# Kernel optimization log

Measured on AMD Instinct MI355X. Metric: run time of the kernel, lower is better.

## Reference

```python
import jax, jax.numpy as jnp
import numpy as np

B, N, D, DK = 8, 2048, 1024, 64
GAMMA = 0.001

def setup_inputs() -> dict:
    key = jax.random.key(0)
    ks = jax.random.split(key, 6)
    x = jax.random.normal(ks[0], (B, N, D), dtype=jnp.float32)
    # nn.Linear weights are [out_features, in_features]; init std=gamma,
    # except fc1/fc2 (modules 4,5) which get std=1e-12 in the original.
    Wq = GAMMA * jax.random.normal(ks[1], (DK, D), dtype=jnp.float32)
    Wk = GAMMA * jax.random.normal(ks[2], (DK, D), dtype=jnp.float32)
    Wv = GAMMA * jax.random.normal(ks[3], (D, D), dtype=jnp.float32)
    W1 = 1e-12 * jax.random.normal(ks[4], (DK, D), dtype=jnp.float32)
    W2 = 1e-12 * jax.random.normal(ks[5], (D, DK), dtype=jnp.float32)
    return {"x": x, "Wq": Wq, "Wk": Wk, "Wv": Wv, "W1": W1, "W2": W2}

def reference(x, Wq, Wk, Wv, W1, W2):
    # Q,K: [B,N,DK]; V: [B,N,D]
    Q = jnp.einsum('bnd,kd->bnk', x, Wq)
    K = jnp.einsum('bnd,kd->bnk', x, Wk)
    V = jnp.einsum('bnd,ed->bne', x, Wv)
    # Linear (non-softmax) attention: (Q @ K^T) @ V
    scores = jnp.einsum('bnk,bmk->bnm', Q, K)      # [B,N,N]
    attention = jnp.einsum('bnm,bme->bne', scores, V)  # [B,N,D]
    x_skip = x + attention
    fc = jnp.einsum('bnd,kd->bnk', x_skip, W1)     # [B,N,DK]
    out = jnp.einsum('bnk,dk->bnd', fc, W2)        # [B,N,D]
    return out
```

## Files before the change

### kernel.cpp

```cpp
#include <hip/hip_runtime.h>

typedef __attribute__((ext_vector_type(8))) __bf16 bf16x8;
typedef __attribute__((ext_vector_type(4))) float f32x4;
typedef unsigned short u16;

#define MFMA16(a, b, c) __builtin_amdgcn_mfma_f32_16x16x32_bf16(a, b, c, 0, 0, 0)

__device__ __forceinline__ u16 f2bf(float f) {
    unsigned u = __float_as_uint(f);
    unsigned r = ((u >> 16) & 1u) + 0x7fffu;
    return (u16)((u + r) >> 16);
}
__device__ __forceinline__ float bf2f(u16 h) {
    return __uint_as_float(((unsigned)h) << 16);
}
__device__ __forceinline__ bf16x8 frag(const u16* base, int rtile, int lane, int kofs) {
    return *(const bf16x8*)(base + (rtile + (lane & 15)) * 72 + kofs + (lane >> 4) * 8);
}

__global__ __launch_bounds__(512) void qkf_kernel(
    const float* __restrict__ x, const float* __restrict__ Wq,
    const float* __restrict__ Wk, const float* __restrict__ W1,
    float* __restrict__ Qp, float* __restrict__ Kp, float* __restrict__ fcp)
{
    __shared__ __align__(16) u16 SM[6 * 4608];
    u16* Xh  = SM;
    u16* Xl  = SM + 4608;
    u16* Wqh = SM + 2 * 4608;
    u16* Wkh = SM + 3 * 4608;
    u16* W1h = SM + 4 * 4608;
    u16* W1l = SM + 5 * 4608;

    const int tid  = threadIdx.x;
    const int lane = tid & 63;
    const int wv   = tid >> 6;
    const int rt   = (wv & 3) * 16;
    const int ch2  = wv >> 2;
    const long row0 = (long)blockIdx.x * 64;
    const int kb   = blockIdx.y * 512;
    const long sOf = (long)blockIdx.y * 1048576;

    const f32x4 zero = {0.f, 0.f, 0.f, 0.f};
    f32x4 qa[2], ka[2], fa[2];
#pragma unroll
    for (int i = 0; i < 2; ++i) { qa[i] = zero; ka[i] = zero; fa[i] = zero; }

    const int sr = tid >> 4;
    const int sk = (tid & 15) * 4;

    float4 xv[2], qv[2], kv[2], w1v[2];
#define QKF_LOAD(K0)                                                          \
    {                                                                         \
        _Pragma("unroll")                                                     \
        for (int i = 0; i < 2; ++i) {                                         \
            int r = sr + i * 32;                                              \
            xv[i]  = *(const float4*)(x  + (row0 + r) * 1024 + (K0) + sk);    \
            qv[i]  = *(const float4*)(Wq + (long)r * 1024 + (K0) + sk);       \
            kv[i]  = *(const float4*)(Wk + (long)r * 1024 + (K0) + sk);       \
            w1v[i] = *(const float4*)(W1 + (long)r * 1024 + (K0) + sk);       \
        }                                                                     \
    }

    QKF_LOAD(kb)
    for (int ch = 0; ch < 8; ++ch) {
        if (ch) __syncthreads();
#pragma unroll
        for (int i = 0; i < 2; ++i) {
            int r = sr + i * 32;
            ushort4 h, l;
            h.x = f2bf(xv[i].x); l.x = f2bf(xv[i].x - bf2f(h.x));
            h.y = f2bf(xv[i].y); l.y = f2bf(xv[i].y - bf2f(h.y));
            h.z = f2bf(xv[i].z); l.z = f2bf(xv[i].z - bf2f(h.z));
            h.w = f2bf(xv[i].w); l.w = f2bf(xv[i].w - bf2f(h.w));
            *(ushort4*)&Xh[r * 72 + sk] = h;
            *(ushort4*)&Xl[r * 72 + sk] = l;
            ushort4 hq;
            hq.x = f2bf(qv[i].x); hq.y = f2bf(qv[i].y);
            hq.z = f2bf(qv[i].z); hq.w = f2bf(qv[i].w);
            *(ushort4*)&Wqh[r * 72 + sk] = hq;
            ushort4 hk;
            hk.x = f2bf(kv[i].x); hk.y = f2bf(kv[i].y);
            hk.z = f2bf(kv[i].z); hk.w = f2bf(kv[i].w);
            *(ushort4*)&Wkh[r * 72 + sk] = hk;
            ushort4 hw, lw;
            hw.x = f2bf(w1v[i].x); lw.x = f2bf(w1v[i].x - bf2f(hw.x));
            hw.y = f2bf(w1v[i].y); lw.y = f2bf(w1v[i].y - bf2f(hw.y));
            hw.z = f2bf(w1v[i].z); lw.z = f2bf(w1v[i].z - bf2f(hw.z));
            hw.w = f2bf(w1v[i].w); lw.w = f2bf(w1v[i].w - bf2f(hw.w));
            *(ushort4*)&W1h[r * 72 + sk] = hw;
            *(ushort4*)&W1l[r * 72 + sk] = lw;
        }
        __syncthreads();
        if (ch < 7) QKF_LOAD(kb + (ch + 1) * 64)
#pragma unroll
        for (int kk = 0; kk < 64; kk += 32) {
            bf16x8 ah = frag(Xh, rt, lane, kk);
            bf16x8 al = frag(Xl, rt, lane, kk);
#pragma unroll
            for (int c = 0; c < 2; ++c) {
                int ct = ch2 * 2 + c;
                qa[c] = MFMA16(ah, frag(Wqh, ct * 16, lane, kk), qa[c]);
                ka[c] = MFMA16(ah, frag(Wkh, ct * 16, lane, kk), ka[c]);
                bf16x8 bh = frag(W1h, ct * 16, lane, kk);
                fa[c] = MFMA16(ah, bh, fa[c]);
                fa[c] = MFMA16(al, bh, fa[c]);
                fa[c] = MFMA16(ah, frag(W1l, ct * 16, lane, kk), fa[c]);
            }
        }
    }
#undef QKF_LOAD

    const int rr = rt + (lane >> 4) * 4;
    const int cc = lane & 15;
#pragma unroll
    for (int c = 0; c < 2; ++c)
#pragma unroll
        for (int g = 0; g < 4; ++g) {
            long o = sOf + (row0 + rr + g) * 64 + (ch2 * 2 + c) * 16 + cc;
            Qp[o]  = qa[c][g];
            Kp[o]  = ka[c][g];
            fcp[o] = fa[c][g];
        }
}

__global__ __launch_bounds__(256) void s_kernel(
    const float* __restrict__ Kp, const float* __restrict__ x,
    float* __restrict__ Sp)
{
    __shared__ __align__(16) u16 Kt[64 * 72];
    __shared__ __align__(16) u16 Xt[64 * 72];

    const int tid = threadIdx.x, lane = tid & 63, wv = tid >> 6;
    const int dt = blockIdx.x, ks = blockIdx.y, b = blockIdx.z;
    const int n0 = ks * 256, d0 = dt * 64;

    const float* Kq = Kp + ((long)b * 2048 + n0) * 64;
    const float* xp = x  + ((long)b * 2048 + n0) * 1024 + d0;

    const f32x4 zero = {0.f, 0.f, 0.f, 0.f};
    f32x4 acc[4];
#pragma unroll
    for (int i = 0; i < 4; ++i) acc[i] = zero;

    float4 kf[4], xv[4];
#define SK_LOAD(NB)                                                           \
    {                                                                         \
        _Pragma("unroll")                                                     \
        for (int i = 0; i < 4; ++i) {                                         \
            float4 a = *(const float4*)(Kq + (long)((NB) + lane) * 64 + wv * 16 + i * 4); \
            float4 c = *(const float4*)(Kq + 1048576 + (long)((NB) + lane) * 64 + wv * 16 + i * 4); \
            kf[i].x = a.x + c.x; kf[i].y = a.y + c.y;                         \
            kf[i].z = a.z + c.z; kf[i].w = a.w + c.w;                         \
            xv[i] = *(const float4*)(xp + (long)((NB) + lane) * 1024 + wv * 16 + i * 4); \
        }                                                                     \
    }

    SK_LOAD(0)
    for (int ch = 0; ch < 4; ++ch) {
        if (ch) __syncthreads();
#pragma unroll
        for (int i = 0; i < 4; ++i) {
            Kt[(wv * 16 + i * 4 + 0) * 72 + lane] = f2bf(kf[i].x);
            Kt[(wv * 16 + i * 4 + 1) * 72 + lane] = f2bf(kf[i].y);
            Kt[(wv * 16 + i * 4 + 2) * 72 + lane] = f2bf(kf[i].z);
            Kt[(wv * 16 + i * 4 + 3) * 72 + lane] = f2bf(kf[i].w);
            Xt[(wv * 16 + i * 4 + 0) * 72 + lane] = f2bf(xv[i].x);
            Xt[(wv * 16 + i * 4 + 1) * 72 + lane] = f2bf(xv[i].y);
            Xt[(wv * 16 + i * 4 + 2) * 72 + lane] = f2bf(xv[i].z);
            Xt[(wv * 16 + i * 4 + 3) * 72 + lane] = f2bf(xv[i].w);
        }
        __syncthreads();
        if (ch < 3) SK_LOAD((ch + 1) * 64)
#pragma unroll
        for (int kk = 0; kk < 64; kk += 32) {
            bf16x8 a = frag(Kt, wv * 16, lane, kk);
#pragma unroll
            for (int ct = 0; ct < 4; ++ct)
                acc[ct] = MFMA16(a, frag(Xt, ct * 16, lane, kk), acc[ct]);
        }
    }
#undef SK_LOAD

    float* C = Sp + ((long)ks * 8 + b) * 65536 + d0;
    const int rr = wv * 16 + (lane >> 4) * 4;
    const int cc = lane & 15;
#pragma unroll
    for (int ct = 0; ct < 4; ++ct)
#pragma unroll
        for (int g = 0; g < 4; ++g)
            C[(long)(rr + g) * 1024 + ct * 16 + cc] = acc[ct][g];
}

template <int AMODE, int BMODE, bool SPLIT, int ASLAB, int BSLAB, int CSLAB>
__global__ __launch_bounds__(256) void mm_nt(
    const void* __restrict__ Ap, int lda, long bsA, long slabA,
    const void* __restrict__ Bp, int ldb, long bsB, long slabB,
    float* __restrict__ Cp, int ldc, long bsC, long splitC,
    const float* __restrict__ Cin, long slabCin,
    int Kred, int nksplit)
{
    __shared__ __align__(16) u16 SMEM[(SPLIT ? 4 : 2) * 4608];
    u16* Ah = SMEM;
    u16* Bh = SMEM + 4608;
    u16* Al = SPLIT ? SMEM + 2 * 4608 : nullptr;
    u16* Bl = SPLIT ? SMEM + 3 * 4608 : nullptr;

    const int tid = threadIdx.x, lane = tid & 63, wv = tid >> 6;
    const int bm = blockIdx.x, bn = blockIdx.y;
    const int batch = blockIdx.z / nksplit;
    const int ks = blockIdx.z % nksplit;
    const int Kper = Kred / nksplit;
    const long kOff = (long)ks * Kper;

    const int r4 = tid >> 4, k4 = (tid & 15) * 4;
    const int r8 = tid >> 3, k8 = (tid & 7) * 8;

    const f32x4 zero = {0.f, 0.f, 0.f, 0.f};
    f32x4 acc[4];
#pragma unroll
    for (int i = 0; i < 4; ++i) acc[i] = zero;

    float4 fva[4], fvb[4];
    uint4  uva[2], uvb[2];
    float  tvb[16];

#define MM_LOADA(K0)                                                          \
    if constexpr (AMODE == 0) {                                               \
        const float* A = (const float*)Ap + (long)batch * bsA                 \
                       + (long)bm * 64 * lda + (K0);                          \
        _Pragma("unroll")                                                     \
        for (int i = 0; i < 4; ++i) {                                         \
            const float* p = A + (long)(r4 + i * 16) * lda + k4;              \
            float4 v = *(const float4*)p;                                     \
            _Pragma("unroll")                                                 \
            for (int s = 1; s < ASLAB; ++s) {                                 \
                float4 w = *(const float4*)(p + (long)s * slabA);             \
                v.x += w.x; v.y += w.y; v.z += w.z; v.w += w.w;               \
            }                                                                 \
            fva[i] = v;                                                       \
        }                                                                     \
    } else {                                                                  \
        const u16* A = (const u16*)Ap + (long)batch * bsA                     \
                     + (long)bm * 64 * lda + (K0);                            \
        _Pragma("unroll")                                                     \
        for (int i = 0; i < 2; ++i)                                           \
            uva[i] = *(const uint4*)(A + (long)(r8 + i * 32) * lda + k8);     \
    }
#define MM_LOADB(K0)                                                          \
    if constexpr (BMODE == 0) {                                               \
        const float* Bq = (const float*)Bp + (long)batch * bsB                \
                        + (long)bn * 64 * ldb + (K0);                         \
        _Pragma("unroll")                                                     \
        for (int i = 0; i < 4; ++i) {                                         \
            const float* p = Bq + (long)(r4 + i * 16) * ldb + k4;             \
            float4 v = *(const float4*)p;                                     \
            _Pragma("unroll")                                                 \
            for (int s = 1; s < BSLAB; ++s) {                                 \
                float4 w = *(const float4*)(p + (long)s * slabB);             \
                v.x += w.x; v.y += w.y; v.z += w.z; v.w += w.w;               \
            }                                                                 \
            fvb[i] = v;                                                       \
        }                                                                     \
    } else if constexpr (BMODE == 1) {                                        \
        const u16* Bq = (const u16*)Bp + (long)batch * bsB                    \
                      + (long)bn * 64 * ldb + (K0);                           \
        _Pragma("unroll")                                                     \
        for (int i = 0; i < 2; ++i)                                           \
            uvb[i] = *(const uint4*)(Bq + (long)(r8 + i * 32) * ldb + k8);    \
    } else {                                                                  \
        const float* Bq = (const float*)Bp + (long)batch * bsB                \
                        + (long)(K0) * ldb + (long)bn * 64;                   \
        _Pragma("unroll")                                                     \
        for (int i = 0; i < 16; ++i)                                          \
            tvb[i] = Bq[(long)((tid >> 6) + i * 4) * ldb + (tid & 63)];       \
    }

    MM_LOADA(kOff) MM_LOADB(kOff)
    for (int k0 = 0; k0 < Kper; k0 += 64) {
        if (k0) __syncthreads();
        if constexpr (AMODE == 0) {
#pragma unroll
            for (int i = 0; i < 4; ++i) {
                int r = r4 + i * 16;
                ushort4 h;
                h.x = f2bf(fva[i].x); h.y = f2bf(fva[i].y);
                h.z = f2bf(fva[i].z); h.w = f2bf(fva[i].w);
                *(ushort4*)&Ah[r * 72 + k4] = h;
                if constexpr (SPLIT) {
                    ushort4 l;
                    l.x = f2bf(fva[i].x - bf2f(h.x)); l.y = f2bf(fva[i].y - bf2f(h.y));
                    l.z = f2bf(fva[i].z - bf2f(h.z)); l.w = f2bf(fva[i].w - bf2f(h.w));
                    *(ushort4*)&Al[r * 72 + k4] = l;
                }
            }
        } else {
#pragma unroll
            for (int i = 0; i < 2; ++i)
                *(uint4*)&Ah[(r8 + i * 32) * 72 + k8] = uva[i];
        }
        if constexpr (BMODE == 0) {
#pragma unroll
            for (int i = 0; i < 4; ++i) {
                int r = r4 + i * 16;
                ushort4 h;
                h.x = f2bf(fvb[i].x); h.y = f2bf(fvb[i].y);
                h.z = f2bf(fvb[i].z); h.w = f2bf(fvb[i].w);
                *(ushort4*)&Bh[r * 72 + k4] = h;
                if constexpr (SPLIT) {
                    ushort4 l;
                    l.x = f2bf(fvb[i].x - bf2f(h.x)); l.y = f2bf(fvb[i].y - bf2f(h.y));
                    l.z = f2bf(fvb[i].z - bf2f(h.z)); l.w = f2bf(fvb[i].w - bf2f(h.w));
                    *(ushort4*)&Bl[r * 72 + k4] = l;
                }
            }
        } else if constexpr (BMODE == 1) {
#pragma unroll
            for (int i = 0; i < 2; ++i)
                *(uint4*)&Bh[(r8 + i * 32) * 72 + k8] = uvb[i];
        } else {
#pragma unroll
            for (int i = 0; i < 16; ++i)
                Bh[(tid & 63) * 72 + (tid >> 6) + i * 4] = f2bf(tvb[i]);
        }
        __syncthreads();
        if (k0 + 64 < Kper) { MM_LOADA(kOff + k0 + 64) MM_LOADB(kOff + k0 + 64) }
#pragma unroll
        for (int kk = 0; kk < 64; kk += 32) {
            bf16x8 ah = frag(Ah, wv * 16, lane, kk);
            bf16x8 al;
            if constexpr (SPLIT) al = frag(Al, wv * 16, lane, kk);
#pragma unroll
            for (int ct = 0; ct < 4; ++ct) {
                bf16x8 bh = frag(Bh, ct * 16, lane, kk);
                acc[ct] = MFMA16(ah, bh, acc[ct]);
                if constexpr (SPLIT) {
                    acc[ct] = MFMA16(al, bh, acc[ct]);
                    acc[ct] = MFMA16(ah, frag(Bl, ct * 16, lane, kk), acc[ct]);
                }
            }
        }
    }
#undef MM_LOADA
#undef MM_LOADB

    const long coff = (long)batch * bsC + (long)bm * 64 * ldc + (long)bn * 64;
    float* C = Cp + coff + (long)ks * splitC;
    const int rr = wv * 16 + (lane >> 4) * 4;
    const int cc = lane & 15;
#pragma unroll
    for (int ct = 0; ct < 4; ++ct)
#pragma unroll
        for (int g = 0; g < 4; ++g) {
            long idx = (long)(rr + g) * ldc + ct * 16 + cc;
            float v = acc[ct][g];
            if constexpr (CSLAB > 0) {
                const float* Ci = Cin + coff + idx;
#pragma unroll
                for (int s = 0; s < CSLAB; ++s) v += Ci[(long)s * slabCin];
            }
            C[idx] = v;
        }
}

extern "C" void kernel_launch(void* const* d_in, const int* in_sizes, int n_in,
                              void* d_out, int out_size, void* d_ws, size_t ws_size,
                              hipStream_t stream)
{
    const float* x  = (const float*)d_in[0];
    const float* Wq = (const float*)d_in[1];
    const float* Wk = (const float*)d_in[2];
    const float* Wv = (const float*)d_in[3];
    const float* W1 = (const float*)d_in[4];
    const float* W2 = (const float*)d_in[5];
    float* out = (float*)d_out;

    const size_t QPB = 8388608, KPB = 8388608, FCPB = 8388608,
                 SPB = 16777216, GPB = 2097152, PBB = 2097152, FCB = 4194304;
    const size_t need = QPB + KPB + FCPB + SPB + GPB + PBB + FCB;

    float *Qp, *Kp, *fcp, *Sp, *Gp, *PBp, *fcb;
    if (ws_size >= need) {
        char* w = (char*)d_ws;
        Qp  = (float*)w;  w += QPB;
        Kp  = (float*)w;  w += KPB;
        fcp = (float*)w;  w += FCPB;
        Sp  = (float*)w;  w += SPB;
        Gp  = (float*)w;  w += GPB;
        PBp = (float*)w;  w += PBB;
        fcb = (float*)w;
    } else {
        char* o = (char*)d_out;
        Qp  = (float*)o;  o += QPB;
        Kp  = (float*)o;  o += KPB;
        fcp = (float*)o;  o += FCPB;
        Sp  = (float*)o;  o += SPB;
        Gp  = (float*)o;  o += GPB;
        PBp = (float*)o;
        fcb = (float*)d_ws;
    }

    qkf_kernel<<<dim3(256, 2), 512, 0, stream>>>(x, Wq, Wk, W1, Qp, Kp, fcp);

    s_kernel<<<dim3(16, 8, 8), 256, 0, stream>>>(Kp, x, Sp);

    mm_nt<0, 2, false, 1, 1, 0><<<dim3(1, 16, 8), 256, 0, stream>>>(
        W1, 1024, 0, 0,   Wv, 1024, 0, 0,
        Gp, 1024, 0, 65536L, nullptr, 0, 1024, 8);

    mm_nt<0, 0, false, 8, 8, 0><<<dim3(1, 1, 128), 256, 0, stream>>>(
        Gp, 1024, 0, 65536L,   Sp, 1024, 65536L, 524288L,
        PBp, 64, 4096L, 32768L, nullptr, 0, 1024, 16);

    mm_nt<0, 0, false, 2, 16, 2><<<dim3(32, 1, 8), 256, 0, stream>>>(
        Qp, 64, 131072L, 1048576L,   PBp, 64, 4096L, 32768L,
        fcb, 64, 131072L, 0, fcp, 1048576L, 64, 1);

    mm_nt<0, 0, true, 1, 1, 0><<<dim3(256, 16, 1), 256, 0, stream>>>(
        fcb, 64, 0, 0,   W2, 64, 0, 0,
        out, 1024, 0, 0, nullptr, 0, 64, 1);
}
```

Before: 213.1 us.

## Use hardware packed bf16 conversion and deepen x prefetch in qkf kernel

Replaces the software round-to-nearest float-to-bf16 routine with the gfx950 v_cvt_pk_bf16_f32 instruction, which converts two floats per instruction in all kernels. The qkf kernel now double-buffers x loads two chunks ahead, unrolled in pairs, so global-load latency has more time to overlap the MFMA work. It also adds an occupancy hint to launch_bounds. The extra register buffers may raise register pressure, and the inline asm depends on the hardware conversion instruction being available.

```diff
diff --git a/kernel.cpp b/kernel.cpp
--- a/kernel.cpp
+++ b/kernel.cpp
@@ -6,19 +6,20 @@
 
 #define MFMA16(a, b, c) __builtin_amdgcn_mfma_f32_16x16x32_bf16(a, b, c, 0, 0, 0)
 
-__device__ __forceinline__ u16 f2bf(float f) {
-    unsigned u = __float_as_uint(f);
-    unsigned r = ((u >> 16) & 1u) + 0x7fffu;
-    return (u16)((u + r) >> 16);
-}
-__device__ __forceinline__ float bf2f(u16 h) {
-    return __uint_as_float(((unsigned)h) << 16);
-}
+__device__ __forceinline__ unsigned cvt2(float a, float b) {
+    unsigned r;
+    asm("v_cvt_pk_bf16_f32 %0, %1, %2" : "=v"(r) : "v"(a), "v"(b));
+    return r;
+}
+__device__ __forceinline__ u16 cvt1(float a) { return (u16)cvt2(a, a); }
+__device__ __forceinline__ float lo2f(unsigned p) { return __uint_as_float(p << 16); }
+__device__ __forceinline__ float hi2f(unsigned p) { return __uint_as_float(p & 0xffff0000u); }
+
 __device__ __forceinline__ bf16x8 frag(const u16* base, int rtile, int lane, int kofs) {
     return *(const bf16x8*)(base + (rtile + (lane & 15)) * 72 + kofs + (lane >> 4) * 8);
 }
 
-__global__ __launch_bounds__(512) void qkf_kernel(
+__global__ __launch_bounds__(512, 4) void qkf_kernel(
     const float* __restrict__ x, const float* __restrict__ Wq,
     const float* __restrict__ Wk, const float* __restrict__ W1,
     float* __restrict__ Qp, float* __restrict__ Kp, float* __restrict__ fcp)
@@ -48,67 +49,79 @@
     const int sr = tid >> 4;
     const int sk = (tid & 15) * 4;
 
-    float4 xv[2], qv[2], kv[2], w1v[2];
-#define QKF_LOAD(K0)                                                          \
-    {                                                                         \
-        _Pragma("unroll")                                                     \
-        for (int i = 0; i < 2; ++i) {                                         \
-            int r = sr + i * 32;                                              \
-            xv[i]  = *(const float4*)(x  + (row0 + r) * 1024 + (K0) + sk);    \
-            qv[i]  = *(const float4*)(Wq + (long)r * 1024 + (K0) + sk);       \
-            kv[i]  = *(const float4*)(Wk + (long)r * 1024 + (K0) + sk);       \
-            w1v[i] = *(const float4*)(W1 + (long)r * 1024 + (K0) + sk);       \
-        }                                                                     \
-    }
-
-    QKF_LOAD(kb)
-    for (int ch = 0; ch < 8; ++ch) {
-        if (ch) __syncthreads();
-#pragma unroll
-        for (int i = 0; i < 2; ++i) {
-            int r = sr + i * 32;
-            ushort4 h, l;
-            h.x = f2bf(xv[i].x); l.x = f2bf(xv[i].x - bf2f(h.x));
-            h.y = f2bf(xv[i].y); l.y = f2bf(xv[i].y - bf2f(h.y));
-            h.z = f2bf(xv[i].z); l.z = f2bf(xv[i].z - bf2f(h.z));
-            h.w = f2bf(xv[i].w); l.w = f2bf(xv[i].w - bf2f(h.w));
-            *(ushort4*)&Xh[r * 72 + sk] = h;
-            *(ushort4*)&Xl[r * 72 + sk] = l;
-            ushort4 hq;
-            hq.x = f2bf(qv[i].x); hq.y = f2bf(qv[i].y);
-            hq.z = f2bf(qv[i].z); hq.w = f2bf(qv[i].w);
-            *(ushort4*)&Wqh[r * 72 + sk] = hq;
-            ushort4 hk;
-            hk.x = f2bf(kv[i].x); hk.y = f2bf(kv[i].y);
-            hk.z = f2bf(kv[i].z); hk.w = f2bf(kv[i].w);
-            *(ushort4*)&Wkh[r * 72 + sk] = hk;
-            ushort4 hw, lw;
-            hw.x = f2bf(w1v[i].x); lw.x = f2bf(w1v[i].x - bf2f(hw.x));
-            hw.y = f2bf(w1v[i].y); lw.y = f2bf(w1v[i].y - bf2f(hw.y));
-            hw.z = f2bf(w1v[i].z); lw.z = f2bf(w1v[i].z - bf2f(hw.z));
-            hw.w = f2bf(w1v[i].w); lw.w = f2bf(w1v[i].w - bf2f(hw.w));
-            *(ushort4*)&W1h[r * 72 + sk] = hw;
-            *(ushort4*)&W1l[r * 72 + sk] = lw;
-        }
+    float4 xv0[2], xv1[2], qv[2], kv[2], w1v[2];
+
+#define LOAD_X(S, K0)                                                         \
+    { _Pragma("unroll")                                                       \
+      for (int i = 0; i < 2; ++i)                                             \
+          xv##S[i] = *(const float4*)(x + (row0 + sr + i * 32) * 1024 + (K0) + sk); }
+#define LOAD_W(K0)                                                            \
+    { _Pragma("unroll")                                                       \
+      for (int i = 0; i < 2; ++i) {                                           \
+          int r = sr + i * 32;                                                \
+          qv[i]  = *(const float4*)(Wq + (long)r * 1024 + (K0) + sk);         \
+          kv[i]  = *(const float4*)(Wk + (long)r * 1024 + (K0) + sk);         \
+          w1v[i] = *(const float4*)(W1 + (long)r * 1024 + (K0) + sk);         \
+      } }
+#define CONV(S)                                                               \
+    { _Pragma("unroll")                                                       \
+      for (int i = 0; i < 2; ++i) {                                           \
+          int r = sr + i * 32;                                                \
+          unsigned xh01 = cvt2(xv##S[i].x, xv##S[i].y);                       \
+          unsigned xh23 = cvt2(xv##S[i].z, xv##S[i].w);                       \
+          unsigned xl01 = cvt2(xv##S[i].x - lo2f(xh01), xv##S[i].y - hi2f(xh01)); \
+          unsigned xl23 = cvt2(xv##S[i].z - lo2f(xh23), xv##S[i].w - hi2f(xh23)); \
+          uint2 t;                                                            \
+          t.x = xh01; t.y = xh23; *(uint2*)&Xh[r * 72 + sk] = t;              \
+          t.x = xl01; t.y = xl23; *(uint2*)&Xl[r * 72 + sk] = t;              \
+          t.x = cvt2(qv[i].x, qv[i].y); t.y = cvt2(qv[i].z, qv[i].w);         \
+          *(uint2*)&Wqh[r * 72 + sk] = t;                                     \
+          t.x = cvt2(kv[i].x, kv[i].y); t.y = cvt2(kv[i].z, kv[i].w);         \
+          *(uint2*)&Wkh[r * 72 + sk] = t;                                     \
+          unsigned wh01 = cvt2(w1v[i].x, w1v[i].y);                           \
+          unsigned wh23 = cvt2(w1v[i].z, w1v[i].w);                           \
+          unsigned wl01 = cvt2(w1v[i].x - lo2f(wh01), w1v[i].y - hi2f(wh01)); \
+          unsigned wl23 = cvt2(w1v[i].z - lo2f(wh23), w1v[i].w - hi2f(wh23)); \
+          t.x = wh01; t.y = wh23; *(uint2*)&W1h[r * 72 + sk] = t;             \
+          t.x = wl01; t.y = wl23; *(uint2*)&W1l[r * 72 + sk] = t;             \
+      } }
+#define MFMA_PHASE                                                            \
+    { _Pragma("unroll")                                                       \
+      for (int kk = 0; kk < 64; kk += 32) {                                   \
+          bf16x8 ah = frag(Xh, rt, lane, kk);                                 \
+          bf16x8 al = frag(Xl, rt, lane, kk);                                 \
+          _Pragma("unroll")                                                   \
+          for (int c = 0; c < 2; ++c) {                                       \
+              int ct = ch2 * 2 + c;                                           \
+              qa[c] = MFMA16(ah, frag(Wqh, ct * 16, lane, kk), qa[c]);        \
+              ka[c] = MFMA16(ah, frag(Wkh, ct * 16, lane, kk), ka[c]);        \
+              bf16x8 bh = frag(W1h, ct * 16, lane, kk);                       \
+              fa[c] = MFMA16(ah, bh, fa[c]);                                  \
+              fa[c] = MFMA16(al, bh, fa[c]);                                  \
+              fa[c] = MFMA16(ah, frag(W1l, ct * 16, lane, kk), fa[c]);        \
+          }                                                                   \
+      } }
+
+    LOAD_X(0, kb) LOAD_X(1, kb + 64) LOAD_W(kb)
+
+    for (int cp = 0; cp < 4; ++cp) {
+        const int kc = kb + cp * 128;
+        if (cp) __syncthreads();
+        CONV(0)
         __syncthreads();
-        if (ch < 7) QKF_LOAD(kb + (ch + 1) * 64)
-#pragma unroll
-        for (int kk = 0; kk < 64; kk += 32) {
-            bf16x8 ah = frag(Xh, rt, lane, kk);
-            bf16x8 al = frag(Xl, rt, lane, kk);
-#pragma unroll
-            for (int c = 0; c < 2; ++c) {
-                int ct = ch2 * 2 + c;
-                qa[c] = MFMA16(ah, frag(Wqh, ct * 16, lane, kk), qa[c]);
-                ka[c] = MFMA16(ah, frag(Wkh, ct * 16, lane, kk), ka[c]);
-                bf16x8 bh = frag(W1h, ct * 16, lane, kk);
-                fa[c] = MFMA16(ah, bh, fa[c]);
-                fa[c] = MFMA16(al, bh, fa[c]);
-                fa[c] = MFMA16(ah, frag(W1l, ct * 16, lane, kk), fa[c]);
-            }
-        }
-    }
-#undef QKF_LOAD
+        if (cp < 3) LOAD_X(0, kc + 128)
+        LOAD_W(kc + 64)
+        MFMA_PHASE
+        __syncthreads();
+        CONV(1)
+        __syncthreads();
+        if (cp < 3) { LOAD_X(1, kc + 192) LOAD_W(kc + 128) }
+        MFMA_PHASE
+    }
+#undef LOAD_X
+#undef LOAD_W
+#undef CONV
+#undef MFMA_PHASE
 
     const int rr = rt + (lane >> 4) * 4;
     const int cc = lane & 15;
@@ -160,14 +173,14 @@
         if (ch) __syncthreads();
 #pragma unroll
         for (int i = 0; i < 4; ++i) {
-            Kt[(wv * 16 + i * 4 + 0) * 72 + lane] = f2bf(kf[i].x);
-            Kt[(wv * 16 + i * 4 + 1) * 72 + lane] = f2bf(kf[i].y);
-            Kt[(wv * 16 + i * 4 + 2) * 72 + lane] = f2bf(kf[i].z);
-            Kt[(wv * 16 + i * 4 + 3) * 72 + lane] = f2bf(kf[i].w);
-            Xt[(wv * 16 + i * 4 + 0) * 72 + lane] = f2bf(xv[i].x);
-            Xt[(wv * 16 + i * 4 + 1) * 72 + lane] = f2bf(xv[i].y);
-            Xt[(wv * 16 + i * 4 + 2) * 72 + lane] = f2bf(xv[i].z);
-            Xt[(wv * 16 + i * 4 + 3) * 72 + lane] = f2bf(xv[i].w);
+            Kt[(wv * 16 + i * 4 + 0) * 72 + lane] = cvt1(kf[i].x);
+            Kt[(wv * 16 + i * 4 + 1) * 72 + lane] = cvt1(kf[i].y);
+            Kt[(wv * 16 + i * 4 + 2) * 72 + lane] = cvt1(kf[i].z);
+            Kt[(wv * 16 + i * 4 + 3) * 72 + lane] = cvt1(kf[i].w);
+            Xt[(wv * 16 + i * 4 + 0) * 72 + lane] = cvt1(xv[i].x);
+            Xt[(wv * 16 + i * 4 + 1) * 72 + lane] = cvt1(xv[i].y);
+            Xt[(wv * 16 + i * 4 + 2) * 72 + lane] = cvt1(xv[i].z);
+            Xt[(wv * 16 + i * 4 + 3) * 72 + lane] = cvt1(xv[i].w);
         }
         __syncthreads();
         if (ch < 3) SK_LOAD((ch + 1) * 64)
@@ -282,15 +295,14 @@
 #pragma unroll
             for (int i = 0; i < 4; ++i) {
                 int r = r4 + i * 16;
-                ushort4 h;
-                h.x = f2bf(fva[i].x); h.y = f2bf(fva[i].y);
-                h.z = f2bf(fva[i].z); h.w = f2bf(fva[i].w);
-                *(ushort4*)&Ah[r * 72 + k4] = h;
+                unsigned h01 = cvt2(fva[i].x, fva[i].y);
+                unsigned h23 = cvt2(fva[i].z, fva[i].w);
+                uint2 t; t.x = h01; t.y = h23;
+                *(uint2*)&Ah[r * 72 + k4] = t;
                 if constexpr (SPLIT) {
-                    ushort4 l;
-                    l.x = f2bf(fva[i].x - bf2f(h.x)); l.y = f2bf(fva[i].y - bf2f(h.y));
-                    l.z = f2bf(fva[i].z - bf2f(h.z)); l.w = f2bf(fva[i].w - bf2f(h.w));
-                    *(ushort4*)&Al[r * 72 + k4] = l;
+                    t.x = cvt2(fva[i].x - lo2f(h01), fva[i].y - hi2f(h01));
+                    t.y = cvt2(fva[i].z - lo2f(h23), fva[i].w - hi2f(h23));
+                    *(uint2*)&Al[r * 72 + k4] = t;
                 }
             }
         } else {
@@ -302,15 +314,14 @@
 #pragma unroll
             for (int i = 0; i < 4; ++i) {
                 int r = r4 + i * 16;
-                ushort4 h;
-                h.x = f2bf(fvb[i].x); h.y = f2bf(fvb[i].y);
-                h.z = f2bf(fvb[i].z); h.w = f2bf(fvb[i].w);
-                *(ushort4*)&Bh[r * 72 + k4] = h;
+                unsigned h01 = cvt2(fvb[i].x, fvb[i].y);
+                unsigned h23 = cvt2(fvb[i].z, fvb[i].w);
+                uint2 t; t.x = h01; t.y = h23;
+                *(uint2*)&Bh[r * 72 + k4] = t;
                 if constexpr (SPLIT) {
-                    ushort4 l;
-                    l.x = f2bf(fvb[i].x - bf2f(h.x)); l.y = f2bf(fvb[i].y - bf2f(h.y));
-                    l.z = f2bf(fvb[i].z - bf2f(h.z)); l.w = f2bf(fvb[i].w - bf2f(h.w));
-                    *(ushort4*)&Bl[r * 72 + k4] = l;
+                    t.x = cvt2(fvb[i].x - lo2f(h01), fvb[i].y - hi2f(h01));
+                    t.y = cvt2(fvb[i].z - lo2f(h23), fvb[i].w - hi2f(h23));
+                    *(uint2*)&Bl[r * 72 + k4] = t;
                 }
             }
         } else if constexpr (BMODE == 1) {
@@ -320,7 +331,7 @@
         } else {
 #pragma unroll
             for (int i = 0; i < 16; ++i)
-                Bh[(tid & 63) * 72 + (tid >> 6) + i * 4] = f2bf(tvb[i]);
+                Bh[(tid & 63) * 72 + (tid >> 6) + i * 4] = cvt1(tvb[i]);
         }
         __syncthreads();
         if (k0 + 64 < Kper) { MM_LOADA(kOff + k0 + 64) MM_LOADB(kOff + k0 + 64) }
```

New measurement: 209.0 us. About the same (-1.9%).
